# Optimization experiments

Measured on AMD Instinct MI355X. Metric: run time of the kernel, lower is better.

## Reference

```python
import jax, jax.numpy as jnp
import numpy as np

B, L, D, V, C = 16384, 50, 128, 91718, 11
H, HD, F = 4, 32, 6
NP = F * (F - 1) // 2  # 15 pairs
CIN = F * D + NP * D   # 2688


def setup_inputs() -> dict:
    key = jax.random.key(0)
    ks = jax.random.split(key, 32)
    inp = {}
    inp['item_id'] = jax.random.randint(ks[0], (B,), 0, V)
    inp['item_mm'] = jax.random.normal(ks[1], (B, D), dtype=jnp.float32)
    inp['likes'] = jax.random.randint(ks[2], (B,), 0, C)
    inp['views'] = jax.random.randint(ks[3], (B,), 0, C)
    inp['item_seq'] = jax.random.randint(ks[4], (B, L), 0, V)
    g = lambda k, shape, s: (jax.random.normal(k, shape, dtype=jnp.float32) * s)
    inp['item_emb'] = g(ks[5], (V, D), 0.02).at[0].set(0.0)  # padding_idx=0
    inp['cate_emb'] = g(ks[6], (C, D), 0.02)
    inp['mm_w'] = g(ks[7], (D, D), (2.0 / D) ** 0.5)
    inp['mm_b'] = jnp.zeros((D,), jnp.float32)
    inp['ln_g'] = jnp.ones((D,), jnp.float32)
    inp['ln_b'] = jnp.zeros((D,), jnp.float32)
    inp['gnn_W'] = g(ks[8], (H, D, HD), (2.0 / (D + HD)) ** 0.5 * 1.414)
    inp['gnn_a'] = g(ks[9], (H, 2 * HD, 1), 0.1)
    inp['se_w1'] = g(ks[10], (F, F // 2), 0.4)
    inp['se_b1'] = jnp.zeros((F // 2,), jnp.float32)
    inp['se_w2'] = g(ks[11], (F // 2, F), 0.4)
    inp['se_b2'] = jnp.zeros((F,), jnp.float32)
    inp['bi_W'] = g(ks[12], (F - 1, D, D), (2.0 / (2 * D)) ** 0.5)
    inp['mlp_w1'] = g(ks[13], (CIN, 512), (2.0 / CIN) ** 0.5)
    inp['mlp_b1'] = jnp.zeros((512,), jnp.float32)
    inp['bn1_g'] = jnp.ones((512,), jnp.float32)
    inp['bn1_b'] = jnp.zeros((512,), jnp.float32)
    inp['mlp_w2'] = g(ks[14], (512, 256), (2.0 / 512) ** 0.5)
    inp['mlp_b2'] = jnp.zeros((256,), jnp.float32)
    inp['bn2_g'] = jnp.ones((256,), jnp.float32)
    inp['bn2_b'] = jnp.zeros((256,), jnp.float32)
    inp['mlp_w3'] = g(ks[15], (256, 1), (2.0 / 256) ** 0.5)
    inp['mlp_b3'] = jnp.zeros((1,), jnp.float32)
    return inp


def _forward(item_id, item_mm, likes, views, item_seq,
             item_emb, cate_emb, mm_w, mm_b, ln_g, ln_b,
             gnn_W, gnn_a, se_w1, se_b1, se_w2, se_b2, bi_W,
             mlp_w1, mlp_b1, bn1_g, bn1_b, mlp_w2, mlp_b2, bn2_g, bn2_b,
             mlp_w3, mlp_b3):
    bsz = item_id.shape[0]
    eps = 1e-5

    user_feat = jnp.zeros((bsz, D), item_mm.dtype)
    like_feat = cate_emb[likes]
    view_feat = cate_emb[views]
    id_feat = item_emb[item_id]

    # mm_proj: Linear -> LayerNorm -> GELU (exact)
    y = item_mm @ mm_w + mm_b
    mu = y.mean(-1, keepdims=True)
    var = y.var(-1, keepdims=True)
    y = (y - mu) * jax.lax.rsqrt(var + eps) * ln_g + ln_b
    img_feat = jax.nn.gelu(y, approximate=False)

    # masked mean pooling of history
    seq_emb = item_emb[item_seq]                          # [B,L,D]
    mask = item_seq == 0
    seq_emb = jnp.where(mask[..., None], 0.0, seq_emb)
    cnt = jnp.clip(jnp.sum((~mask).astype(seq_emb.dtype), axis=1, keepdims=True), 1.0)
    hist_feat = seq_emb.sum(1) / cnt

    x = jnp.stack([user_feat, like_feat, view_feat, id_feat, img_feat, hist_feat], axis=1)  # [B,6,D]

    # GAT over 6-node fully-connected feature graph
    hp = jnp.einsum('bni,hio->bnho', x, gnn_W)            # [B,6,H,HD]
    a1 = gnn_a[:, :HD, 0]                                  # [H,HD]
    a2 = gnn_a[:, HD:, 0]
    ei = jnp.einsum('bnhd,hd->bhn', hp, a1)
    ej = jnp.einsum('bnhd,hd->bhn', hp, a2)
    e = ei[:, :, :, None] + ej[:, :, None, :]             # [B,H,6,6]
    e = jnp.where(e > 0, e, 0.2 * e)                       # LeakyReLU(0.2)
    att = jax.nn.softmax(e, axis=-1)                       # dropout off (eval)
    h_new = jnp.einsum('bhnm,bmho->bnho', att, hp).reshape(bsz, F, D)
    gnn_feat = jax.nn.elu(h_new + x)                       # in_dim == out_dim

    # SENet
    z = gnn_feat.mean(-1)                                  # [B,6]
    w = jax.nn.sigmoid(jax.nn.relu(z @ se_w1 + se_b1) @ se_w2 + se_b2)
    s = gnn_feat * w[..., None]

    # Bilinear ('each'): vid_i = s_i @ W_i, pairs (i,j), j>i
    vid = jnp.einsum('bfd,fde->bfe', s[:, :F - 1], bi_W)   # [B,5,D]
    p = jnp.stack([vid[:, i] * s[:, j] for i in range(F - 1) for j in range(i + 1, F)], axis=1)  # [B,15,D]

    c = jnp.concatenate([gnn_feat.reshape(bsz, -1), p.reshape(bsz, -1)], axis=1)  # [B,2688]

    # MLP with eval-mode BatchNorm (running mean 0, var 1) and dropout off
    bn = lambda t, g_, b_: t * (g_ / jnp.sqrt(1.0 + eps)) + b_
    h1 = jax.nn.gelu(bn(c @ mlp_w1 + mlp_b1, bn1_g, bn1_b), approximate=False)
    h2 = jax.nn.gelu(bn(h1 @ mlp_w2 + mlp_b2, bn2_g, bn2_b), approximate=False)
    out = jax.nn.sigmoid(h2 @ mlp_w3 + mlp_b3)
    return out.squeeze(-1)


def reference(item_id, item_mm, likes, views, item_seq,
              item_emb, cate_emb, mm_w, mm_b, ln_g, ln_b,
              gnn_W, gnn_a, se_w1, se_b1, se_w2, se_b2, bi_W,
              mlp_w1, mlp_b1, bn1_g, bn1_b, mlp_w2, mlp_b2, bn2_g, bn2_b,
              mlp_w3, mlp_b3):
    return _forward(item_id, item_mm, likes, views, item_seq,
                    item_emb, cate_emb, mm_w, mm_b, ln_g, ln_b,
                    gnn_W, gnn_a, se_w1, se_b1, se_w2, se_b2, bi_W,
                    mlp_w1, mlp_b1, bn1_g, bn1_b, mlp_w2, mlp_b2, bn2_g, bn2_b,
                    mlp_w3, mlp_b3)
```

## Files before the change

### kernel.cpp

```cpp
#include <hip/hip_runtime.h>
#include <hip/hip_bf16.h>
#include <cstdint>
#include <cstddef>

#define BB 16384

typedef float  floatx4 __attribute__((ext_vector_type(4)));
typedef __bf16 bf16x8  __attribute__((ext_vector_type(8)));

__device__ __forceinline__ unsigned short f2bf(float f) {
  union { float f; unsigned int u; } v; v.f = f;
  unsigned int r = v.u + 0x7FFFu + ((v.u >> 16) & 1u);
  return (unsigned short)(r >> 16);
}
__device__ __forceinline__ float bf2f(unsigned short h) {
  union { unsigned int u; float f; } v; v.u = ((unsigned int)h) << 16;
  return v.f;
}
__device__ __forceinline__ float gelu_exact(float x) {
  return 0.5f * x * (1.0f + erff(x * 0.7071067811865475f));
}

#define ALOAD16(g, l) \
  __builtin_amdgcn_global_load_lds((const __attribute__((address_space(1))) void*)(g), \
                                   (__attribute__((address_space(3))) void*)(l), 16, 0, 0)

__global__ void k_pack(const float* __restrict__ mm_w, const float* __restrict__ gnn_W,
                       const float* __restrict__ bi_W, const float* __restrict__ item_mm,
                       const float* __restrict__ item_emb,
                       unsigned short* __restrict__ mmwt, unsigned short* __restrict__ wallt,
                       unsigned short* __restrict__ biwt, unsigned short* __restrict__ immb,
                       unsigned short* __restrict__ iembb)
{
  const int total = 2211840 + 2934976;
  for (int id = blockIdx.x * 256 + threadIdx.x; id < total; id += gridDim.x * 256) {
    if (id < 16384) {
      int n = id / 128, k = id % 128;
      mmwt[id] = f2bf(mm_w[k * 128 + n]);
    } else if (id < 32768) {
      int l = id - 16384; int nc = l / 128, k = l % 128;
      wallt[l] = f2bf(gnn_W[(nc >> 5) * 4096 + k * 32 + (nc & 31)]);
    } else if (id < 114688) {
      int l = id - 32768; int f = l / 16384, rr = l % 16384, e = rr / 128, d = rr % 128;
      biwt[l] = f2bf(bi_W[f * 16384 + d * 128 + e]);
    } else if (id < 2211840) {
      int l = id - 114688;
      immb[l] = f2bf(item_mm[l]);
    } else {
      int l = id - 2211840;
      float4 v = ((const float4*)item_emb)[l];
      ushort4 o; o.x = f2bf(v.x); o.y = f2bf(v.y); o.z = f2bf(v.z); o.w = f2bf(v.w);
      ((ushort4*)iembb)[l] = o;
    }
  }
}

__global__ __launch_bounds__(256)
void k_transp(const float* __restrict__ in, unsigned short* __restrict__ out, int R, int C)
{
  __shared__ float tile[64][65];
  const int c0 = blockIdx.x * 64, r0 = blockIdx.y * 64;
  const int lr = threadIdx.x >> 6;
  const int lc = threadIdx.x & 63;
  #pragma unroll
  for (int i = 0; i < 16; i++) {
    int r = lr + i * 4;
    tile[r][lc] = in[(size_t)(r0 + r) * C + c0 + lc];
  }
  __syncthreads();
  #pragma unroll
  for (int i = 0; i < 16; i++) {
    int c = lr + i * 4;
    out[(size_t)(c0 + c) * R + r0 + lc] = f2bf(tile[lc][c]);
  }
}

template<int BM, int EPI, bool SWZ>
__global__ __launch_bounds__(512)
void gemm_bt(const unsigned short* __restrict__ A, int lda,
             const unsigned short* __restrict__ Bt, int ldb,
             void* __restrict__ Cp, int ldc, int K,
             const float* __restrict__ bias, const float* __restrict__ bng,
             const float* __restrict__ bnb)
{
  constexpr int WGM = BM / 64;
  constexpr int WGN = 8 / WGM;
  constexpr int TN  = 128 / WGN;
  constexpr int NT  = TN / 16;
  constexpr int NRW = (BM + 128) / 8;
  constexpr int ISS = NRW / 8;

  int bx = blockIdx.x, by = blockIdx.y;
  if constexpr (SWZ) {
    int p = by * gridDim.x + bx;
    int xcd = p & 7, slot = p >> 3;
    bx = slot % gridDim.x;
    by = xcd * (gridDim.y >> 3) + slot / gridDim.x;
  }
  const int n0 = bx * 128;
  const int m0 = by * BM;
  __shared__ __align__(16) unsigned short As[BM * 64];
  __shared__ __align__(16) unsigned short Bs[128 * 64];
  const int t = threadIdx.x;
  const int lane = t & 63, w = t >> 6;
  const int wm = w % WGM, wn = w / WGM;
  const int lr = lane & 15, lq = lane >> 4;

  floatx4 acc[4][NT];
  #pragma unroll
  for (int a = 0; a < 4; a++)
    #pragma unroll
    for (int b = 0; b < NT; b++) acc[a][b] = (floatx4){0.f, 0.f, 0.f, 0.f};

  const int srow = lane >> 3;
  const int schk = (lane & 7) ^ srow;
  const int rb0 = w * NRW;

  for (int k0 = 0; k0 < K; k0 += 64) {
    __syncthreads();
    #pragma unroll
    for (int q = 0; q < ISS; q++) {
      const int rb = rb0 + q * 8;
      if (rb < BM) {
        ALOAD16(A + (size_t)(m0 + rb + srow) * lda + k0 + schk * 8, As + rb * 64);
      } else {
        const int rbb = rb - BM;
        ALOAD16(Bt + (size_t)(n0 + rbb + srow) * ldb + k0 + schk * 8, Bs + rbb * 64);
      }
    }
    __syncthreads();
    #pragma unroll
    for (int ko = 0; ko < 2; ko++) {
      bf16x8 af[4], bfv[NT];
      #pragma unroll
      for (int mt = 0; mt < 4; mt++) {
        const int row = wm * 64 + mt * 16 + lr;
        const int pc = (ko * 4 + lq) ^ (lr & 7);
        af[mt] = __builtin_bit_cast(bf16x8, *(const uint4*)&As[row * 64 + pc * 8]);
      }
      #pragma unroll
      for (int nt = 0; nt < NT; nt++) {
        const int row = wn * TN + nt * 16 + lr;
        const int pc = (ko * 4 + lq) ^ (lr & 7);
        bfv[nt] = __builtin_bit_cast(bf16x8, *(const uint4*)&Bs[row * 64 + pc * 8]);
      }
      #pragma unroll
      for (int mt = 0; mt < 4; mt++)
        #pragma unroll
        for (int nt = 0; nt < NT; nt++)
          acc[mt][nt] = __builtin_amdgcn_mfma_f32_16x16x32_bf16(af[mt], bfv[nt], acc[mt][nt], 0, 0, 0);
    }
  }

  #pragma unroll
  for (int mt = 0; mt < 4; mt++)
    #pragma unroll
    for (int nt = 0; nt < NT; nt++)
      #pragma unroll
      for (int i = 0; i < 4; i++) {
        const int cm = m0 + wm * 64 + mt * 16 + lq * 4 + i;
        const int cn = n0 + wn * TN + nt * 16 + lr;
        float v = acc[mt][nt][i];
        size_t idx = (size_t)cm * ldc + cn;
        if constexpr (EPI == 0) {
          ((float*)Cp)[idx] = v + bias[cn];
        } else if constexpr (EPI == 2) {
          ((unsigned short*)Cp)[idx] = f2bf(v);
        } else {
          float tt = v + bias[cn];
          tt = tt * (bng[cn] * 0.9999950000374997f) + bnb[cn];
          ((unsigned short*)Cp)[idx] = f2bf(gelu_exact(tt));
        }
      }
}

__global__ __launch_bounds__(256)
void gemm_vid(const unsigned short* __restrict__ sbb, const unsigned short* __restrict__ biwt,
              unsigned short* __restrict__ c)
{
  const int z = blockIdx.z;
  const int m0 = blockIdx.y * 128;
  __shared__ __align__(16) unsigned short smem[128 * 130];
  unsigned short* As = smem;
  unsigned short* Bs = smem + 8192;
  const int t = threadIdx.x;
  const int lane = t & 63, w = t >> 6;
  const int wm = w & 1, wn = w >> 1;
  const int lr = lane & 15, lq = lane >> 4;

  floatx4 acc[4][4];
  #pragma unroll
  for (int a = 0; a < 4; a++)
    #pragma unroll
    for (int b = 0; b < 4; b++) acc[a][b] = (floatx4){0.f, 0.f, 0.f, 0.f};

  const int srow = lane >> 3;
  const int schk = (lane & 7) ^ srow;
  const unsigned short* Ag = sbb + (size_t)(m0 + w * 32 + srow) * 768 + z * 128 + schk * 8;
  const unsigned short* Bg = biwt + z * 16384 + (size_t)(w * 32 + srow) * 128 + schk * 8;
  unsigned short* AsW = As + w * 32 * 64;
  unsigned short* BsW = Bs + w * 32 * 64;

  for (int k0 = 0; k0 < 128; k0 += 64) {
    __syncthreads();
    #pragma unroll
    for (int q = 0; q < 4; q++) {
      ALOAD16(Ag + k0 + (size_t)(q * 8) * 768, AsW + q * 512);
      ALOAD16(Bg + k0 + (size_t)(q * 8) * 128, BsW + q * 512);
    }
    __syncthreads();
    #pragma unroll
    for (int ko = 0; ko < 2; ko++) {
      bf16x8 af[4], bfv[4];
      #pragma unroll
      for (int mt = 0; mt < 4; mt++) {
        const int row = wm * 64 + mt * 16 + lr;
        const int pc = (ko * 4 + lq) ^ (lr & 7);
        af[mt] = __builtin_bit_cast(bf16x8, *(const uint4*)&As[row * 64 + pc * 8]);
      }
      #pragma unroll
      for (int nt = 0; nt < 4; nt++) {
        const int row = wn * 64 + nt * 16 + lr;
        const int pc = (ko * 4 + lq) ^ (lr & 7);
        bfv[nt] = __builtin_bit_cast(bf16x8, *(const uint4*)&Bs[row * 64 + pc * 8]);
      }
      #pragma unroll
      for (int mt = 0; mt < 4; mt++)
        #pragma unroll
        for (int nt = 0; nt < 4; nt++)
          acc[mt][nt] = __builtin_amdgcn_mfma_f32_16x16x32_bf16(af[mt], bfv[nt], acc[mt][nt], 0, 0, 0);
    }
  }

  __syncthreads();
  #pragma unroll
  for (int mt = 0; mt < 4; mt++)
    #pragma unroll
    for (int nt = 0; nt < 4; nt++)
      #pragma unroll
      for (int i = 0; i < 4; i++) {
        const int rr = wm * 64 + mt * 16 + lq * 4 + i;
        const int cc = wn * 64 + nt * 16 + lr;
        smem[rr * 130 + cc] = f2bf(acc[mt][nt][i]);
      }
  __syncthreads();

  const int pb0[5] = {0, 5, 9, 12, 14};
  const int npairs = 5 - z;
  const int tot = 128 * 32 * npairs;
  for (int e = t; e < tot; e += 256) {
    const int g  = e & 31;
    const int rp = e >> 5;
    const int p  = rp % npairs;
    const int r  = rp / npairs;
    ushort4 vv = *(const ushort4*)&smem[r * 130 + g * 4];
    ushort4 sv = *(const ushort4*)&sbb[(size_t)(m0 + r) * 768 + (z + 1 + p) * 128 + g * 4];
    ushort4 o;
    o.x = f2bf(bf2f(vv.x) * bf2f(sv.x));
    o.y = f2bf(bf2f(vv.y) * bf2f(sv.y));
    o.z = f2bf(bf2f(vv.z) * bf2f(sv.z));
    o.w = f2bf(bf2f(vv.w) * bf2f(sv.w));
    *(ushort4*)&c[(size_t)(m0 + r) * 2688 + 768 + (size_t)(pb0[z] + p) * 128 + g * 4] = o;
  }
}

__global__ __launch_bounds__(256)
void k_feat(const int* __restrict__ item_id, const int* __restrict__ likes,
            const int* __restrict__ views, const int* __restrict__ item_seq,
            const unsigned short* __restrict__ iembb, const float* __restrict__ cate_emb,
            unsigned short* __restrict__ xb)
{
  const int b = blockIdx.x * 4 + (threadIdx.x >> 6);
  const int lane = threadIdx.x & 63;
  const int half = lane >> 5, ql = lane & 31;
  const size_t base = (size_t)b * 768;
  const int li = likes[b], vi = views[b], id = item_id[b];

  int idxs[25];
  #pragma unroll
  for (int j = 0; j < 25; j++) idxs[j] = item_seq[b * 50 + half + 2 * j];

  float4 hs = make_float4(0.f, 0.f, 0.f, 0.f);
  float cnt = 0.f;
  #pragma unroll
  for (int j = 0; j < 25; j++) {
    const int idx = idxs[j];
    if (idx != 0) {
      cnt += 1.0f;
      ushort4 v = *(const ushort4*)&iembb[(size_t)idx * 128 + ql * 4];
      hs.x += bf2f(v.x); hs.y += bf2f(v.y); hs.z += bf2f(v.z); hs.w += bf2f(v.w);
    }
  }
  cnt  += __shfl_xor(cnt, 32, 64);
  hs.x += __shfl_xor(hs.x, 32, 64);
  hs.y += __shfl_xor(hs.y, 32, 64);
  hs.z += __shfl_xor(hs.z, 32, 64);
  hs.w += __shfl_xor(hs.w, 32, 64);
  const float ic = 1.0f / fmaxf(cnt, 1.0f);

  *(unsigned int*)&xb[base + lane * 2] = 0u;

  {
    const float4 v = *(const float4*)&cate_emb[(size_t)(half ? vi : li) * 128 + ql * 4];
    ushort4 o; o.x = f2bf(v.x); o.y = f2bf(v.y); o.z = f2bf(v.z); o.w = f2bf(v.w);
    *(ushort4*)&xb[base + 128 + half * 128 + ql * 4] = o;
  }
  if (half == 0) {
    *(ushort4*)&xb[base + 384 + ql * 4] =
        *(const ushort4*)&iembb[(size_t)id * 128 + ql * 4];
  } else {
    ushort4 o; o.x = f2bf(hs.x * ic); o.y = f2bf(hs.y * ic);
               o.z = f2bf(hs.z * ic); o.w = f2bf(hs.w * ic);
    *(ushort4*)&xb[base + 640 + ql * 4] = o;
  }
}

__global__ __launch_bounds__(256)
void k_ln(const float* __restrict__ y, const float* __restrict__ ln_g,
          const float* __restrict__ ln_b, unsigned short* __restrict__ xb)
{
  const int b = blockIdx.x * 4 + (threadIdx.x >> 6);
  const int lane = threadIdx.x & 63;
  float v0 = y[(size_t)b * 128 + lane], v1 = y[(size_t)b * 128 + lane + 64];
  float s = v0 + v1, s2 = v0 * v0 + v1 * v1;
  #pragma unroll
  for (int o = 32; o > 0; o >>= 1) { s += __shfl_xor(s, o, 64); s2 += __shfl_xor(s2, o, 64); }
  float mu  = s * (1.0f / 128.0f);
  float var = s2 * (1.0f / 128.0f) - mu * mu;
  float rs  = rsqrtf(var + 1e-5f);
  float t0 = (v0 - mu) * rs * ln_g[lane]      + ln_b[lane];
  float t1 = (v1 - mu) * rs * ln_g[lane + 64] + ln_b[lane + 64];
  xb[(size_t)b * 768 + 512 + lane]      = f2bf(gelu_exact(t0));
  xb[(size_t)b * 768 + 512 + lane + 64] = f2bf(gelu_exact(t1));
}

__global__ __launch_bounds__(256)
void k_att(const unsigned short* __restrict__ hp, const unsigned short* __restrict__ xb,
           const float* __restrict__ gnn_a, const float* __restrict__ se_w1,
           const float* __restrict__ se_b1, const float* __restrict__ se_w2,
           const float* __restrict__ se_b2, unsigned short* __restrict__ c,
           unsigned short* __restrict__ sb)
{
  __shared__ float hps[4][6][128];
  __shared__ float eis[4][4][6], ejs[4][4][6];
  __shared__ float atts[4][4][6][6];
  const int wv = threadIdx.x >> 6, lane = threadIdx.x & 63;
  const int b = blockIdx.x * 4 + wv;

  #pragma unroll
  for (int n = 0; n < 6; n++) {
    unsigned int pk = *(const unsigned int*)&hp[((size_t)b * 6 + n) * 128 + lane * 2];
    float2 f; f.x = bf2f((unsigned short)(pk & 0xFFFFu));
              f.y = bf2f((unsigned short)(pk >> 16));
    *(float2*)&hps[wv][n][lane * 2] = f;
  }
  __syncthreads();

  if (lane < 24) {
    int h = lane & 3, n = lane >> 2;
    float e1 = 0.f, e2 = 0.f;
    for (int o = 0; o < 32; o++) {
      float v = hps[wv][n][h * 32 + o];
      e1 += v * gnn_a[h * 64 + o];
      e2 += v * gnn_a[h * 64 + 32 + o];
    }
    eis[wv][h][n] = e1; ejs[wv][h][n] = e2;
  }
  __syncthreads();

  if (lane < 24) {
    int h = lane & 3, i = lane >> 2;
    float ev[6]; float mx = -1e30f;
    #pragma unroll
    for (int j = 0; j < 6; j++) {
      float e = eis[wv][h][i] + ejs[wv][h][j];
      e = e > 0.f ? e : 0.2f * e;
      ev[j] = e; mx = fmaxf(mx, e);
    }
    float ssum = 0.f;
    #pragma unroll
    for (int j = 0; j < 6; j++) { ev[j] = expf(ev[j] - mx); ssum += ev[j]; }
    float inv = 1.0f / ssum;
    #pragma unroll
    for (int j = 0; j < 6; j++) atts[wv][h][i][j] = ev[j] * inv;
  }
  __syncthreads();

  const int h = lane >> 4;
  float g0[6], g1[6], zz[6];
  #pragma unroll
  for (int n = 0; n < 6; n++) {
    float hn0 = 0.f, hn1 = 0.f;
    #pragma unroll
    for (int m = 0; m < 6; m++) {
      float a = atts[wv][h][n][m];
      float2 v = *(const float2*)&hps[wv][m][lane * 2];
      hn0 += a * v.x; hn1 += a * v.y;
    }
    unsigned int xp = *(const unsigned int*)&xb[(size_t)b * 768 + n * 128 + lane * 2];
    float a0 = hn0 + bf2f((unsigned short)(xp & 0xFFFFu));
    float a1 = hn1 + bf2f((unsigned short)(xp >> 16));
    a0 = a0 > 0.f ? a0 : expm1f(a0);
    a1 = a1 > 0.f ? a1 : expm1f(a1);
    g0[n] = a0; g1[n] = a1;
    float zacc = a0 + a1;
    #pragma unroll
    for (int o = 32; o > 0; o >>= 1) zacc += __shfl_xor(zacc, o, 64);
    zz[n] = zacc * (1.0f / 128.0f);
  }

  float rr[3];
  #pragma unroll
  for (int j = 0; j < 3; j++) {
    float a = se_b1[j];
    #pragma unroll
    for (int n = 0; n < 6; n++) a += zz[n] * se_w1[n * 3 + j];
    rr[j] = fmaxf(a, 0.f);
  }
  float wse[6];
  #pragma unroll
  for (int n = 0; n < 6; n++) {
    float a = se_b2[n];
    #pragma unroll
    for (int j = 0; j < 3; j++) a += rr[j] * se_w2[j * 6 + n];
    wse[n] = 1.0f / (1.0f + expf(-a));
  }

  #pragma unroll
  for (int n = 0; n < 6; n++) {
    unsigned int pc = (unsigned int)f2bf(g0[n]) | ((unsigned int)f2bf(g1[n]) << 16);
    unsigned int ps = (unsigned int)f2bf(g0[n] * wse[n]) | ((unsigned int)f2bf(g1[n] * wse[n]) << 16);
    *(unsigned int*)&c[(size_t)b * 2688 + n * 128 + lane * 2]  = pc;
    *(unsigned int*)&sb[(size_t)b * 768 + n * 128 + lane * 2]  = ps;
  }
}

__global__ __launch_bounds__(256)
void k_out(const unsigned short* __restrict__ h2, const float* __restrict__ w3,
           const float* __restrict__ b3, float* __restrict__ out)
{
  const int b = blockIdx.x * 4 + (threadIdx.x >> 6);
  const int lane = threadIdx.x & 63;
  ushort4 v = *(const ushort4*)&h2[(size_t)b * 256 + lane * 4];
  float a = bf2f(v.x) * w3[lane * 4]     + bf2f(v.y) * w3[lane * 4 + 1]
          + bf2f(v.z) * w3[lane * 4 + 2] + bf2f(v.w) * w3[lane * 4 + 3];
  #pragma unroll
  for (int o = 32; o > 0; o >>= 1) a += __shfl_xor(a, o, 64);
  if (lane == 0) out[b] = 1.0f / (1.0f + expf(-(a + b3[0])));
}

#define OFF_MMWT   0ull
#define OFF_WALLT  32768ull
#define OFF_BIWT   65536ull
#define OFF_W1T    229376ull
#define OFF_W2T    2981888ull
#define OFF_IMMB   3244032ull
#define OFF_XB     7438336ull
#define OFF_HP     32604160ull
#define OFF_SB     57769984ull
#define OFF_C      82935808ull
#define OFF_H2     171016192ull
#define OFF_IEMB   179404800ull

extern "C" void kernel_launch(void* const* d_in, const int* in_sizes, int n_in,
                              void* d_out, int out_size, void* d_ws, size_t ws_size,
                              hipStream_t stream)
{
  const int*   item_id  = (const int*)  d_in[0];
  const float* item_mm  = (const float*)d_in[1];
  const int*   likes    = (const int*)  d_in[2];
  const int*   views    = (const int*)  d_in[3];
  const int*   item_seq = (const int*)  d_in[4];
  const float* item_emb = (const float*)d_in[5];
  const float* cate_emb = (const float*)d_in[6];
  const float* mm_w     = (const float*)d_in[7];
  const float* mm_b     = (const float*)d_in[8];
  const float* ln_g     = (const float*)d_in[9];
  const float* ln_b     = (const float*)d_in[10];
  const float* gnn_W    = (const float*)d_in[11];
  const float* gnn_a    = (const float*)d_in[12];
  const float* se_w1    = (const float*)d_in[13];
  const float* se_b1    = (const float*)d_in[14];
  const float* se_w2    = (const float*)d_in[15];
  const float* se_b2    = (const float*)d_in[16];
  const float* bi_W     = (const float*)d_in[17];
  const float* mlp_w1   = (const float*)d_in[18];
  const float* mlp_b1   = (const float*)d_in[19];
  const float* bn1_g    = (const float*)d_in[20];
  const float* bn1_b    = (const float*)d_in[21];
  const float* mlp_w2   = (const float*)d_in[22];
  const float* mlp_b2   = (const float*)d_in[23];
  const float* bn2_g    = (const float*)d_in[24];
  const float* bn2_b    = (const float*)d_in[25];
  const float* mlp_w3   = (const float*)d_in[26];
  const float* mlp_b3   = (const float*)d_in[27];
  float* out = (float*)d_out;

  char* ws = (char*)d_ws;
  unsigned short* mmwt  = (unsigned short*)(ws + OFF_MMWT);
  unsigned short* wallt = (unsigned short*)(ws + OFF_WALLT);
  unsigned short* biwt  = (unsigned short*)(ws + OFF_BIWT);
  unsigned short* w1t   = (unsigned short*)(ws + OFF_W1T);
  unsigned short* w2t   = (unsigned short*)(ws + OFF_W2T);
  unsigned short* immb  = (unsigned short*)(ws + OFF_IMMB);
  unsigned short* xb    = (unsigned short*)(ws + OFF_XB);
  unsigned short* hpb   = (unsigned short*)(ws + OFF_HP);
  unsigned short* sbb   = (unsigned short*)(ws + OFF_SB);
  float*          yb    = (float*)         (ws + OFF_SB);
  unsigned short* cbuf  = (unsigned short*)(ws + OFF_C);
  unsigned short* h1b   = (unsigned short*)(ws + OFF_XB);
  unsigned short* h2b   = (unsigned short*)(ws + OFF_H2);
  unsigned short* iembb = (unsigned short*)(ws + OFF_IEMB);

  k_pack<<<4096, 256, 0, stream>>>(mm_w, gnn_W, bi_W, item_mm, item_emb,
                                   mmwt, wallt, biwt, immb, iembb);
  k_transp<<<dim3(8, 42), 256, 0, stream>>>(mlp_w1, w1t, 2688, 512);
  k_transp<<<dim3(4, 8),  256, 0, stream>>>(mlp_w2, w2t, 512, 256);
  k_feat<<<BB / 4, 256, 0, stream>>>(item_id, likes, views, item_seq, iembb, cate_emb, xb);
  gemm_bt<64, 0, false><<<dim3(1, 256), 512, 0, stream>>>(immb, 128, mmwt, 128,
      yb, 128, 128, mm_b, nullptr, nullptr);
  k_ln<<<BB / 4, 256, 0, stream>>>(yb, ln_g, ln_b, xb);
  gemm_bt<128, 2, false><<<dim3(1, 768), 512, 0, stream>>>(xb, 128, wallt, 128,
      hpb, 128, 128, nullptr, nullptr, nullptr);
  k_att<<<BB / 4, 256, 0, stream>>>(hpb, xb, gnn_a, se_w1, se_b1, se_w2, se_b2, cbuf, sbb);
  gemm_vid<<<dim3(1, 128, 5), 256, 0, stream>>>(sbb, biwt, cbuf);
  gemm_bt<128, 3, true><<<dim3(4, 128), 512, 0, stream>>>(cbuf, 2688, w1t, 2688,
      h1b, 512, 2688, mlp_b1, bn1_g, bn1_b);
  gemm_bt<64, 3, true><<<dim3(2, 256), 512, 0, stream>>>(h1b, 512, w2t, 512,
      h2b, 256, 512, mlp_b2, bn2_g, bn2_b);
  k_out<<<BB / 4, 256, 0, stream>>>(h2b, mlp_w3, mlp_b3, out);
}
```

Before: 349.6 us.

## Fuse small GEMMs with LayerNorm, GAT attention, and output epilogues

Merges the mm projection GEMM with LayerNorm+GELU, the GNN head projection GEMM with the attention/SE block, and the second MLP GEMM with the final dot-product sigmoid. The two weight transposes are also combined into one launch. Intermediate tensors (y, hp, h2) now stay in LDS instead of making a global round trip, and several launches are removed. In exchange each fused kernel does a serialized epilogue after its GEMM, uses more shared memory per block, and runs fewer blocks.

```diff
diff --git a/kernel.cpp b/kernel.cpp
--- a/kernel.cpp
+++ b/kernel.cpp
@@ -56,10 +56,15 @@
 }
 
 __global__ __launch_bounds__(256)
-void k_transp(const float* __restrict__ in, unsigned short* __restrict__ out, int R, int C)
+void k_transp2(const float* __restrict__ w1, const float* __restrict__ w2,
+               unsigned short* __restrict__ w1t, unsigned short* __restrict__ w2t)
 {
   __shared__ float tile[64][65];
-  const int c0 = blockIdx.x * 64, r0 = blockIdx.y * 64;
+  int blk = blockIdx.x;
+  const float* in; unsigned short* outp; int R, C, bx, by;
+  if (blk < 336) { in = w1; outp = w1t; R = 2688; C = 512; bx = blk % 8; by = blk / 8; }
+  else { blk -= 336; in = w2; outp = w2t; R = 512; C = 256; bx = blk % 4; by = blk / 4; }
+  const int c0 = bx * 64, r0 = by * 64;
   const int lr = threadIdx.x >> 6;
   const int lc = threadIdx.x & 63;
   #pragma unroll
@@ -71,7 +76,7 @@
   #pragma unroll
   for (int i = 0; i < 16; i++) {
     int c = lr + i * 4;
-    out[(size_t)(c0 + c) * R + r0 + lc] = f2bf(tile[lc][c]);
+    outp[(size_t)(c0 + c) * R + r0 + lc] = f2bf(tile[lc][c]);
   }
 }
 
@@ -162,16 +167,248 @@
         const int cn = n0 + wn * TN + nt * 16 + lr;
         float v = acc[mt][nt][i];
         size_t idx = (size_t)cm * ldc + cn;
-        if constexpr (EPI == 0) {
-          ((float*)Cp)[idx] = v + bias[cn];
-        } else if constexpr (EPI == 2) {
-          ((unsigned short*)Cp)[idx] = f2bf(v);
-        } else {
-          float tt = v + bias[cn];
-          tt = tt * (bng[cn] * 0.9999950000374997f) + bnb[cn];
-          ((unsigned short*)Cp)[idx] = f2bf(gelu_exact(tt));
-        }
-      }
+        float tt = v + bias[cn];
+        tt = tt * (bng[cn] * 0.9999950000374997f) + bnb[cn];
+        ((unsigned short*)Cp)[idx] = f2bf(gelu_exact(tt));
+      }
+}
+
+__global__ __launch_bounds__(512)
+void k_mmln(const unsigned short* __restrict__ A, const unsigned short* __restrict__ Bt,
+            const float* __restrict__ mm_b, const float* __restrict__ ln_g,
+            const float* __restrict__ ln_b, unsigned short* __restrict__ xb)
+{
+  __shared__ __align__(16) char smem[64 * 130 * 4];
+  unsigned short* As = (unsigned short*)smem;
+  unsigned short* Bs = (unsigned short*)(smem + 8192);
+  float* cls = (float*)smem;
+
+  const int t = threadIdx.x, lane = t & 63, w = t >> 6;
+  const int lr = lane & 15, lq = lane >> 4;
+  const int m0 = blockIdx.x * 64;
+
+  floatx4 acc[4];
+  #pragma unroll
+  for (int a = 0; a < 4; a++) acc[a] = (floatx4){0.f, 0.f, 0.f, 0.f};
+
+  const int srow = lane >> 3;
+  const int schk = (lane & 7) ^ srow;
+  const int rb0 = w * 24;
+
+  for (int k0 = 0; k0 < 128; k0 += 64) {
+    __syncthreads();
+    #pragma unroll
+    for (int q = 0; q < 3; q++) {
+      const int rb = rb0 + q * 8;
+      if (rb < 64) ALOAD16(A + (size_t)(m0 + rb + srow) * 128 + k0 + schk * 8, As + rb * 64);
+      else { const int rbb = rb - 64; ALOAD16(Bt + (size_t)(rbb + srow) * 128 + k0 + schk * 8, Bs + rbb * 64); }
+    }
+    __syncthreads();
+    #pragma unroll
+    for (int ko = 0; ko < 2; ko++) {
+      bf16x8 af[4], bv;
+      #pragma unroll
+      for (int mt = 0; mt < 4; mt++) {
+        const int row = mt * 16 + lr;
+        const int pc = (ko * 4 + lq) ^ (lr & 7);
+        af[mt] = __builtin_bit_cast(bf16x8, *(const uint4*)&As[row * 64 + pc * 8]);
+      }
+      {
+        const int row = w * 16 + lr;
+        const int pc = (ko * 4 + lq) ^ (lr & 7);
+        bv = __builtin_bit_cast(bf16x8, *(const uint4*)&Bs[row * 64 + pc * 8]);
+      }
+      #pragma unroll
+      for (int mt = 0; mt < 4; mt++)
+        acc[mt] = __builtin_amdgcn_mfma_f32_16x16x32_bf16(af[mt], bv, acc[mt], 0, 0, 0);
+    }
+  }
+
+  __syncthreads();
+  #pragma unroll
+  for (int mt = 0; mt < 4; mt++)
+    #pragma unroll
+    for (int i = 0; i < 4; i++) {
+      const int rr = mt * 16 + lq * 4 + i;
+      const int cc = w * 16 + lr;
+      cls[rr * 130 + cc] = acc[mt][i] + mm_b[cc];
+    }
+  __syncthreads();
+
+  const float2 g2 = *(const float2*)&ln_g[lane * 2];
+  const float2 b2 = *(const float2*)&ln_b[lane * 2];
+  #pragma unroll
+  for (int rr = 0; rr < 8; rr++) {
+    const int r = w * 8 + rr;
+    float2 v = *(const float2*)&cls[r * 130 + lane * 2];
+    float s = v.x + v.y, s2 = v.x * v.x + v.y * v.y;
+    #pragma unroll
+    for (int o = 32; o > 0; o >>= 1) { s += __shfl_xor(s, o, 64); s2 += __shfl_xor(s2, o, 64); }
+    float mu  = s * (1.0f / 128.0f);
+    float var = s2 * (1.0f / 128.0f) - mu * mu;
+    float rs  = rsqrtf(var + 1e-5f);
+    float t0 = gelu_exact((v.x - mu) * rs * g2.x + b2.x);
+    float t1 = gelu_exact((v.y - mu) * rs * g2.y + b2.y);
+    unsigned int pk = (unsigned int)f2bf(t0) | ((unsigned int)f2bf(t1) << 16);
+    *(unsigned int*)&xb[(size_t)(m0 + r) * 768 + 512 + lane * 2] = pk;
+  }
+}
+
+__global__ __launch_bounds__(256)
+void k_hpatt(const unsigned short* __restrict__ xb, const unsigned short* __restrict__ wallt,
+             const float* __restrict__ gnn_a, const float* __restrict__ se_w1,
+             const float* __restrict__ se_b1, const float* __restrict__ se_w2,
+             const float* __restrict__ se_b2, unsigned short* __restrict__ c,
+             unsigned short* __restrict__ sb)
+{
+  __shared__ __align__(16) char smem[52992];
+  unsigned short* As = (unsigned short*)smem;
+  unsigned short* Bs = (unsigned short*)(smem + 12288);
+  float* hps  = (float*)smem;
+  float* eis  = (float*)(smem + 49920);
+  float* ejs  = eis + 96;
+  float* atts = ejs + 96;
+
+  const int t = threadIdx.x, lane = t & 63, w = t >> 6;
+  const int wm = w & 1, wn = w >> 1;
+  const int lr = lane & 15, lq = lane >> 4;
+  const int m0 = blockIdx.x * 96;
+
+  floatx4 acc[3][4];
+  #pragma unroll
+  for (int a = 0; a < 3; a++)
+    #pragma unroll
+    for (int b = 0; b < 4; b++) acc[a][b] = (floatx4){0.f, 0.f, 0.f, 0.f};
+
+  const int srow = lane >> 3;
+  const int schk = (lane & 7) ^ srow;
+  const int rb0 = w * 56;
+
+  for (int k0 = 0; k0 < 128; k0 += 64) {
+    __syncthreads();
+    #pragma unroll
+    for (int q = 0; q < 7; q++) {
+      const int rb = rb0 + q * 8;
+      if (rb < 96) ALOAD16(xb + (size_t)(m0 + rb + srow) * 128 + k0 + schk * 8, As + rb * 64);
+      else { const int rbb = rb - 96; ALOAD16(wallt + (size_t)(rbb + srow) * 128 + k0 + schk * 8, Bs + rbb * 64); }
+    }
+    __syncthreads();
+    #pragma unroll
+    for (int ko = 0; ko < 2; ko++) {
+      bf16x8 af[3], bfv[4];
+      #pragma unroll
+      for (int mt = 0; mt < 3; mt++) {
+        const int row = wm * 48 + mt * 16 + lr;
+        const int pc = (ko * 4 + lq) ^ (lr & 7);
+        af[mt] = __builtin_bit_cast(bf16x8, *(const uint4*)&As[row * 64 + pc * 8]);
+      }
+      #pragma unroll
+      for (int nt = 0; nt < 4; nt++) {
+        const int row = wn * 64 + nt * 16 + lr;
+        const int pc = (ko * 4 + lq) ^ (lr & 7);
+        bfv[nt] = __builtin_bit_cast(bf16x8, *(const uint4*)&Bs[row * 64 + pc * 8]);
+      }
+      #pragma unroll
+      for (int mt = 0; mt < 3; mt++)
+        #pragma unroll
+        for (int nt = 0; nt < 4; nt++)
+          acc[mt][nt] = __builtin_amdgcn_mfma_f32_16x16x32_bf16(af[mt], bfv[nt], acc[mt][nt], 0, 0, 0);
+    }
+  }
+
+  __syncthreads();
+  #pragma unroll
+  for (int mt = 0; mt < 3; mt++)
+    #pragma unroll
+    for (int nt = 0; nt < 4; nt++)
+      #pragma unroll
+      for (int i = 0; i < 4; i++) {
+        const int rr = wm * 48 + mt * 16 + lq * 4 + i;
+        const int cc = wn * 64 + nt * 16 + lr;
+        hps[rr * 130 + cc] = acc[mt][nt][i];
+      }
+  __syncthreads();
+
+  for (int it = 0; it < 4; it++) {
+    const int lb = w * 4 + it;
+    const int b = blockIdx.x * 16 + lb;
+    const float* hb = hps + lb * 6 * 130;
+
+    if (lane < 24) {
+      int h = lane & 3, n = lane >> 2;
+      float e1 = 0.f, e2 = 0.f;
+      for (int o = 0; o < 32; o++) {
+        float v = hb[n * 130 + h * 32 + o];
+        e1 += v * gnn_a[h * 64 + o];
+        e2 += v * gnn_a[h * 64 + 32 + o];
+      }
+      eis[w * 24 + h * 6 + n] = e1; ejs[w * 24 + h * 6 + n] = e2;
+    }
+    if (lane < 24) {
+      int h = lane & 3, i = lane >> 2;
+      float ev[6]; float mx = -1e30f;
+      #pragma unroll
+      for (int j = 0; j < 6; j++) {
+        float e = eis[w * 24 + h * 6 + i] + ejs[w * 24 + h * 6 + j];
+        e = e > 0.f ? e : 0.2f * e;
+        ev[j] = e; mx = fmaxf(mx, e);
+      }
+      float ssum = 0.f;
+      #pragma unroll
+      for (int j = 0; j < 6; j++) { ev[j] = expf(ev[j] - mx); ssum += ev[j]; }
+      float inv = 1.0f / ssum;
+      #pragma unroll
+      for (int j = 0; j < 6; j++) atts[w * 144 + h * 36 + i * 6 + j] = ev[j] * inv;
+    }
+
+    const int hh = lane >> 4;
+    float g0[6], g1[6], zz[6];
+    #pragma unroll
+    for (int n = 0; n < 6; n++) {
+      float hn0 = 0.f, hn1 = 0.f;
+      #pragma unroll
+      for (int m = 0; m < 6; m++) {
+        float a = atts[w * 144 + hh * 36 + n * 6 + m];
+        float2 v = *(const float2*)&hb[m * 130 + lane * 2];
+        hn0 += a * v.x; hn1 += a * v.y;
+      }
+      unsigned int xp = *(const unsigned int*)&xb[(size_t)b * 768 + n * 128 + lane * 2];
+      float a0 = hn0 + bf2f((unsigned short)(xp & 0xFFFFu));
+      float a1 = hn1 + bf2f((unsigned short)(xp >> 16));
+      a0 = a0 > 0.f ? a0 : expm1f(a0);
+      a1 = a1 > 0.f ? a1 : expm1f(a1);
+      g0[n] = a0; g1[n] = a1;
+      float zacc = a0 + a1;
+      #pragma unroll
+      for (int o = 32; o > 0; o >>= 1) zacc += __shfl_xor(zacc, o, 64);
+      zz[n] = zacc * (1.0f / 128.0f);
+    }
+
+    float rr3[3];
+    #pragma unroll
+    for (int j = 0; j < 3; j++) {
+      float a = se_b1[j];
+      #pragma unroll
+      for (int n = 0; n < 6; n++) a += zz[n] * se_w1[n * 3 + j];
+      rr3[j] = fmaxf(a, 0.f);
+    }
+    float wse[6];
+    #pragma unroll
+    for (int n = 0; n < 6; n++) {
+      float a = se_b2[n];
+      #pragma unroll
+      for (int j = 0; j < 3; j++) a += rr3[j] * se_w2[j * 6 + n];
+      wse[n] = 1.0f / (1.0f + expf(-a));
+    }
+
+    #pragma unroll
+    for (int n = 0; n < 6; n++) {
+      unsigned int pc = (unsigned int)f2bf(g0[n]) | ((unsigned int)f2bf(g1[n]) << 16);
+      unsigned int ps = (unsigned int)f2bf(g0[n] * wse[n]) | ((unsigned int)f2bf(g1[n] * wse[n]) << 16);
+      *(unsigned int*)&c[(size_t)b * 2688 + n * 128 + lane * 2]  = pc;
+      *(unsigned int*)&sb[(size_t)b * 768 + n * 128 + lane * 2]  = ps;
+    }
+  }
 }
 
 __global__ __launch_bounds__(256)
@@ -315,138 +552,88 @@
   }
 }
 
-__global__ __launch_bounds__(256)
-void k_ln(const float* __restrict__ y, const float* __restrict__ ln_g,
-          const float* __restrict__ ln_b, unsigned short* __restrict__ xb)
-{
-  const int b = blockIdx.x * 4 + (threadIdx.x >> 6);
-  const int lane = threadIdx.x & 63;
-  float v0 = y[(size_t)b * 128 + lane], v1 = y[(size_t)b * 128 + lane + 64];
-  float s = v0 + v1, s2 = v0 * v0 + v1 * v1;
-  #pragma unroll
-  for (int o = 32; o > 0; o >>= 1) { s += __shfl_xor(s, o, 64); s2 += __shfl_xor(s2, o, 64); }
-  float mu  = s * (1.0f / 128.0f);
-  float var = s2 * (1.0f / 128.0f) - mu * mu;
-  float rs  = rsqrtf(var + 1e-5f);
-  float t0 = (v0 - mu) * rs * ln_g[lane]      + ln_b[lane];
-  float t1 = (v1 - mu) * rs * ln_g[lane + 64] + ln_b[lane + 64];
-  xb[(size_t)b * 768 + 512 + lane]      = f2bf(gelu_exact(t0));
-  xb[(size_t)b * 768 + 512 + lane + 64] = f2bf(gelu_exact(t1));
-}
-
-__global__ __launch_bounds__(256)
-void k_att(const unsigned short* __restrict__ hp, const unsigned short* __restrict__ xb,
-           const float* __restrict__ gnn_a, const float* __restrict__ se_w1,
-           const float* __restrict__ se_b1, const float* __restrict__ se_w2,
-           const float* __restrict__ se_b2, unsigned short* __restrict__ c,
-           unsigned short* __restrict__ sb)
-{
-  __shared__ float hps[4][6][128];
-  __shared__ float eis[4][4][6], ejs[4][4][6];
-  __shared__ float atts[4][4][6][6];
-  const int wv = threadIdx.x >> 6, lane = threadIdx.x & 63;
-  const int b = blockIdx.x * 4 + wv;
-
-  #pragma unroll
-  for (int n = 0; n < 6; n++) {
-    unsigned int pk = *(const unsigned int*)&hp[((size_t)b * 6 + n) * 128 + lane * 2];
-    float2 f; f.x = bf2f((unsigned short)(pk & 0xFFFFu));
-              f.y = bf2f((unsigned short)(pk >> 16));
-    *(float2*)&hps[wv][n][lane * 2] = f;
-  }
-  __syncthreads();
-
-  if (lane < 24) {
-    int h = lane & 3, n = lane >> 2;
-    float e1 = 0.f, e2 = 0.f;
-    for (int o = 0; o < 32; o++) {
-      float v = hps[wv][n][h * 32 + o];
-      e1 += v * gnn_a[h * 64 + o];
-      e2 += v * gnn_a[h * 64 + 32 + o];
-    }
-    eis[wv][h][n] = e1; ejs[wv][h][n] = e2;
-  }
-  __syncthreads();
-
-  if (lane < 24) {
-    int h = lane & 3, i = lane >> 2;
-    float ev[6]; float mx = -1e30f;
-    #pragma unroll
-    for (int j = 0; j < 6; j++) {
-      float e = eis[wv][h][i] + ejs[wv][h][j];
-      e = e > 0.f ? e : 0.2f * e;
-      ev[j] = e; mx = fmaxf(mx, e);
-    }
-    float ssum = 0.f;
-    #pragma unroll
-    for (int j = 0; j < 6; j++) { ev[j] = expf(ev[j] - mx); ssum += ev[j]; }
-    float inv = 1.0f / ssum;
-    #pragma unroll
-    for (int j = 0; j < 6; j++) atts[wv][h][i][j] = ev[j] * inv;
-  }
-  __syncthreads();
-
-  const int h = lane >> 4;
-  float g0[6], g1[6], zz[6];
-  #pragma unroll
-  for (int n = 0; n < 6; n++) {
-    float hn0 = 0.f, hn1 = 0.f;
-    #pragma unroll
-    for (int m = 0; m < 6; m++) {
-      float a = atts[wv][h][n][m];
-      float2 v = *(const float2*)&hps[wv][m][lane * 2];
-      hn0 += a * v.x; hn1 += a * v.y;
-    }
-    unsigned int xp = *(const unsigned int*)&xb[(size_t)b * 768 + n * 128 + lane * 2];
-    float a0 = hn0 + bf2f((unsigned short)(xp & 0xFFFFu));
-    float a1 = hn1 + bf2f((unsigned short)(xp >> 16));
-    a0 = a0 > 0.f ? a0 : expm1f(a0);
-    a1 = a1 > 0.f ? a1 : expm1f(a1);
-    g0[n] = a0; g1[n] = a1;
-    float zacc = a0 + a1;
-    #pragma unroll
-    for (int o = 32; o > 0; o >>= 1) zacc += __shfl_xor(zacc, o, 64);
-    zz[n] = zacc * (1.0f / 128.0f);
-  }
-
-  float rr[3];
-  #pragma unroll
-  for (int j = 0; j < 3; j++) {
-    float a = se_b1[j];
-    #pragma unroll
-    for (int n = 0; n < 6; n++) a += zz[n] * se_w1[n * 3 + j];
-    rr[j] = fmaxf(a, 0.f);
-  }
-  float wse[6];
-  #pragma unroll
-  for (int n = 0; n < 6; n++) {
-    float a = se_b2[n];
-    #pragma unroll
-    for (int j = 0; j < 3; j++) a += rr[j] * se_w2[j * 6 + n];
-    wse[n] = 1.0f / (1.0f + expf(-a));
-  }
-
-  #pragma unroll
-  for (int n = 0; n < 6; n++) {
-    unsigned int pc = (unsigned int)f2bf(g0[n]) | ((unsigned int)f2bf(g1[n]) << 16);
-    unsigned int ps = (unsigned int)f2bf(g0[n] * wse[n]) | ((unsigned int)f2bf(g1[n] * wse[n]) << 16);
-    *(unsigned int*)&c[(size_t)b * 2688 + n * 128 + lane * 2]  = pc;
-    *(unsigned int*)&sb[(size_t)b * 768 + n * 128 + lane * 2]  = ps;
-  }
-}
-
-__global__ __launch_bounds__(256)
-void k_out(const unsigned short* __restrict__ h2, const float* __restrict__ w3,
-           const float* __restrict__ b3, float* __restrict__ out)
-{
-  const int b = blockIdx.x * 4 + (threadIdx.x >> 6);
-  const int lane = threadIdx.x & 63;
-  ushort4 v = *(const ushort4*)&h2[(size_t)b * 256 + lane * 4];
-  float a = bf2f(v.x) * w3[lane * 4]     + bf2f(v.y) * w3[lane * 4 + 1]
-          + bf2f(v.z) * w3[lane * 4 + 2] + bf2f(v.w) * w3[lane * 4 + 3];
-  #pragma unroll
-  for (int o = 32; o > 0; o >>= 1) a += __shfl_xor(a, o, 64);
-  if (lane == 0) out[b] = 1.0f / (1.0f + expf(-(a + b3[0])));
+__global__ __launch_bounds__(512)
+void k_mlp2out(const unsigned short* __restrict__ A, const unsigned short* __restrict__ Bt,
+               const float* __restrict__ b2v, const float* __restrict__ bng,
+               const float* __restrict__ bnb, const float* __restrict__ w3,
+               const float* __restrict__ b3, float* __restrict__ out)
+{
+  __shared__ __align__(16) char smem[40960];
+  unsigned short* As = (unsigned short*)smem;
+  unsigned short* Bs = (unsigned short*)(smem + 8192);
+  unsigned short* h2s = (unsigned short*)smem;
+
+  const int t = threadIdx.x, lane = t & 63, w = t >> 6;
+  const int lr = lane & 15, lq = lane >> 4;
+  const int m0 = blockIdx.x * 64;
+
+  floatx4 acc[4][2];
+  #pragma unroll
+  for (int a = 0; a < 4; a++)
+    #pragma unroll
+    for (int b = 0; b < 2; b++) acc[a][b] = (floatx4){0.f, 0.f, 0.f, 0.f};
+
+  const int srow = lane >> 3;
+  const int schk = (lane & 7) ^ srow;
+  const int rb0 = w * 40;
+
+  for (int k0 = 0; k0 < 512; k0 += 64) {
+    __syncthreads();
+    #pragma unroll
+    for (int q = 0; q < 5; q++) {
+      const int rb = rb0 + q * 8;
+      if (rb < 64) ALOAD16(A + (size_t)(m0 + rb + srow) * 512 + k0 + schk * 8, As + rb * 64);
+      else { const int rbb = rb - 64; ALOAD16(Bt + (size_t)(rbb + srow) * 512 + k0 + schk * 8, Bs + rbb * 64); }
+    }
+    __syncthreads();
+    #pragma unroll
+    for (int ko = 0; ko < 2; ko++) {
+      bf16x8 af[4], bfv[2];
+      #pragma unroll
+      for (int mt = 0; mt < 4; mt++) {
+        const int row = mt * 16 + lr;
+        const int pc = (ko * 4 + lq) ^ (lr & 7);
+        af[mt] = __builtin_bit_cast(bf16x8, *(const uint4*)&As[row * 64 + pc * 8]);
+      }
+      #pragma unroll
+      for (int nt = 0; nt < 2; nt++) {
+        const int row = w * 32 + nt * 16 + lr;
+        const int pc = (ko * 4 + lq) ^ (lr & 7);
+        bfv[nt] = __builtin_bit_cast(bf16x8, *(const uint4*)&Bs[row * 64 + pc * 8]);
+      }
+      #pragma unroll
+      for (int mt = 0; mt < 4; mt++)
+        #pragma unroll
+        for (int nt = 0; nt < 2; nt++)
+          acc[mt][nt] = __builtin_amdgcn_mfma_f32_16x16x32_bf16(af[mt], bfv[nt], acc[mt][nt], 0, 0, 0);
+    }
+  }
+
+  __syncthreads();
+  #pragma unroll
+  for (int mt = 0; mt < 4; mt++)
+    #pragma unroll
+    for (int nt = 0; nt < 2; nt++)
+      #pragma unroll
+      for (int i = 0; i < 4; i++) {
+        const int rr = mt * 16 + lq * 4 + i;
+        const int cc = w * 32 + nt * 16 + lr;
+        float tt = acc[mt][nt][i] + b2v[cc];
+        tt = tt * (bng[cc] * 0.9999950000374997f) + bnb[cc];
+        h2s[rr * 264 + cc] = f2bf(gelu_exact(tt));
+      }
+  __syncthreads();
+
+  const float4 w4 = *(const float4*)&w3[lane * 4];
+  #pragma unroll
+  for (int rr = 0; rr < 8; rr++) {
+    const int r = w * 8 + rr;
+    ushort4 v = *(const ushort4*)&h2s[r * 264 + lane * 4];
+    float a = bf2f(v.x) * w4.x + bf2f(v.y) * w4.y + bf2f(v.z) * w4.z + bf2f(v.w) * w4.w;
+    #pragma unroll
+    for (int o = 32; o > 0; o >>= 1) a += __shfl_xor(a, o, 64);
+    if (lane == 0) out[m0 + r] = 1.0f / (1.0f + expf(-(a + b3[0])));
+  }
 }
 
 #define OFF_MMWT   0ull
@@ -456,10 +643,8 @@
 #define OFF_W2T    2981888ull
 #define OFF_IMMB   3244032ull
 #define OFF_XB     7438336ull
-#define OFF_HP     32604160ull
 #define OFF_SB     57769984ull
 #define OFF_C      82935808ull
-#define OFF_H2     171016192ull
 #define OFF_IEMB   179404800ull
 
 extern "C" void kernel_launch(void* const* d_in, const int* in_sizes, int n_in,
@@ -504,29 +689,19 @@
   unsigned short* w2t   = (unsigned short*)(ws + OFF_W2T);
   unsigned short* immb  = (unsigned short*)(ws + OFF_IMMB);
   unsigned short* xb    = (unsigned short*)(ws + OFF_XB);
-  unsigned short* hpb   = (unsigned short*)(ws + OFF_HP);
   unsigned short* sbb   = (unsigned short*)(ws + OFF_SB);
-  float*          yb    = (float*)         (ws + OFF_SB);
   unsigned short* cbuf  = (unsigned short*)(ws + OFF_C);
   unsigned short* h1b   = (unsigned short*)(ws + OFF_XB);
-  unsigned short* h2b   = (unsigned short*)(ws + OFF_H2);
   unsigned short* iembb = (unsigned short*)(ws + OFF_IEMB);
 
   k_pack<<<4096, 256, 0, stream>>>(mm_w, gnn_W, bi_W, item_mm, item_emb,
                                    mmwt, wallt, biwt, immb, iembb);
-  k_transp<<<dim3(8, 42), 256, 0, stream>>>(mlp_w1, w1t, 2688, 512);
-  k_transp<<<dim3(4, 8),  256, 0, stream>>>(mlp_w2, w2t, 512, 256);
+  k_transp2<<<368, 256, 0, stream>>>(mlp_w1, mlp_w2, w1t, w2t);
   k_feat<<<BB / 4, 256, 0, stream>>>(item_id, likes, views, item_seq, iembb, cate_emb, xb);
-  gemm_bt<64, 0, false><<<dim3(1, 256), 512, 0, stream>>>(immb, 128, mmwt, 128,
-      yb, 128, 128, mm_b, nullptr, nullptr);
-  k_ln<<<BB / 4, 256, 0, stream>>>(yb, ln_g, ln_b, xb);
-  gemm_bt<128, 2, false><<<dim3(1, 768), 512, 0, stream>>>(xb, 128, wallt, 128,
-      hpb, 128, 128, nullptr, nullptr, nullptr);
-  k_att<<<BB / 4, 256, 0, stream>>>(hpb, xb, gnn_a, se_w1, se_b1, se_w2, se_b2, cbuf, sbb);
+  k_mmln<<<256, 512, 0, stream>>>(immb, mmwt, mm_b, ln_g, ln_b, xb);
+  k_hpatt<<<1024, 256, 0, stream>>>(xb, wallt, gnn_a, se_w1, se_b1, se_w2, se_b2, cbuf, sbb);
   gemm_vid<<<dim3(1, 128, 5), 256, 0, stream>>>(sbb, biwt, cbuf);
   gemm_bt<128, 3, true><<<dim3(4, 128), 512, 0, stream>>>(cbuf, 2688, w1t, 2688,
       h1b, 512, 2688, mlp_b1, bn1_g, bn1_b);
-  gemm_bt<64, 3, true><<<dim3(2, 256), 512, 0, stream>>>(h1b, 512, w2t, 512,
-      h2b, 256, 512, mlp_b2, bn2_g, bn2_b);
-  k_out<<<BB / 4, 256, 0, stream>>>(h2b, mlp_w3, mlp_b3, out);
-}
+  k_mlp2out<<<256, 512, 0, stream>>>(h1b, w2t, mlp_b2, bn2_g, bn2_b, mlp_w3, mlp_b3, out);
+}
```

Result: no change. 347.2 us (-0.7%).
